# Performance work log

Measured on AMD Instinct MI355X. Metric: run time of the kernel, lower is better.

The kernel has to match this reference:

```python
import jax, jax.numpy as jnp
import numpy as np

N = 100000          # nodes
E = 1600000         # edges
DIMS = [128, 64, 64, 47]  # in_feats -> hidden -> hidden -> n_classes
EPS = 1e-5


def setup_inputs() -> dict:
    key = jax.random.key(0)
    ks = jax.random.split(key, 10)
    d = {
        "features": jax.random.normal(ks[0], (N, DIMS[0]), jnp.float32),
        "src": jax.random.randint(ks[1], (E,), 0, N, dtype=jnp.int64),
        "dst": jax.random.randint(ks[2], (E,), 0, N, dtype=jnp.int64),
    }
    # GraphConv weights (glorot-ish) + bias
    for i in range(3):
        fan_in, fan_out = DIMS[i], DIMS[i + 1]
        scale = jnp.sqrt(2.0 / (fan_in + fan_out)).astype(jnp.float32)
        d[f"W{i}"] = jax.random.normal(ks[3 + i], (fan_in, fan_out), jnp.float32) * scale
        d[f"b{i}"] = jnp.zeros((fan_out,), jnp.float32)
    # BatchNorm affine params for the first two layers
    for i in range(2):
        d[f"gamma{i}"] = jnp.ones((DIMS[i + 1],), jnp.float32)
        d[f"beta{i}"] = jnp.zeros((DIMS[i + 1],), jnp.float32)
    return d


def _degree_isqrt(idx):
    # clamp degree to >=1 like DGL, then D^{-1/2}
    deg = jax.ops.segment_sum(jnp.ones((E,), jnp.float32), idx, num_segments=N)
    return jax.lax.rsqrt(jnp.maximum(deg, 1.0))


def _graph_conv(h, W, b, src, dst, out_isqrt, in_isqrt):
    # DGL GraphConv, norm='both': h' = D_in^{-1/2} A D_out^{-1/2} h W + b
    h = h * out_isqrt[:, None]
    if W.shape[0] > W.shape[1]:  # mult W first when it shrinks features (DGL order)
        h = h @ W
        h = jax.ops.segment_sum(h[src], dst, num_segments=N)
    else:
        h = jax.ops.segment_sum(h[src], dst, num_segments=N)
        h = h @ W
    return h * in_isqrt[:, None] + b


def _batch_norm(h, gamma, beta):
    mu = h.mean(axis=0)
    var = h.var(axis=0)  # biased, as torch BatchNorm uses for normalization
    return gamma * (h - mu) * jax.lax.rsqrt(var + EPS) + beta


def reference(features, src, dst, W0, b0, W1, b1, W2, b2,
              gamma0, beta0, gamma1, beta1):
    out_isqrt = _degree_isqrt(src)
    in_isqrt = _degree_isqrt(dst)
    Ws = [(W0, b0), (W1, b1), (W2, b2)]
    bns = [(gamma0, beta0), (gamma1, beta1)]
    h = features
    for i, (W, b) in enumerate(Ws):
        # dropout (p=0.5) before last layer only -> identity in eval mode
        h = _graph_conv(h, W, b, src, dst, out_isqrt, in_isqrt)
        if i < len(Ws) - 1:
            h = _batch_norm(h, *bns[i])
            h = jax.nn.relu(h)
    return h
```

## Files before the change

kernel.cpp:

```cpp
#include <hip/hip_runtime.h>
#include <hip/hip_bf16.h>
#include <hip/hip_fp16.h>

#define BN_EPS 1e-5f
#define N_MAX 100000
#define CAP 64
#define NB_MAX 391
#define BCAP 8192

__device__ float g_wsf[130 * N_MAX + 256];
__device__ int   g_wsi[(1 + CAP) * N_MAX + NB_MAX * BCAP + 2 * NB_MAX + 64];
__device__ unsigned char g_wsb[NB_MAX * BCAP];

__global__ __launch_bounds__(256)
void k_bin(const int* __restrict__ src, const int* __restrict__ dst,
           int* __restrict__ gcur, int* __restrict__ scur,
           int* __restrict__ pairs, unsigned char* __restrict__ sbytes,
           int E, int nb) {
    __shared__ int dh[NB_MAX], db[NB_MAX], dc[NB_MAX];
    __shared__ int sh[NB_MAX], sb[NB_MAX], sc[NB_MAX];
    const int tid = threadIdx.x;
    for (int i = tid; i < nb; i += 256) { dh[i] = 0; sh[i] = 0; dc[i] = 0; sc[i] = 0; }
    __syncthreads();
    const int e0 = blockIdx.x * 4096;
    int ss[16], dd[16];
#pragma unroll
    for (int i = 0; i < 16; ++i) {
        int e = e0 + i * 256 + tid;
        if (e < E) {
            ss[i] = src[e]; dd[i] = dst[e];
            atomicAdd(&dh[dd[i] >> 8], 1);
            atomicAdd(&sh[ss[i] >> 8], 1);
        } else ss[i] = -1;
    }
    __syncthreads();
    for (int i = tid; i < nb; i += 256) {
        db[i] = atomicAdd(&gcur[i], dh[i]);
        sb[i] = atomicAdd(&scur[i], sh[i]);
    }
    __syncthreads();
#pragma unroll
    for (int i = 0; i < 16; ++i) {
        if (ss[i] >= 0) {
            int b = dd[i] >> 8;
            int idx = db[b] + atomicAdd(&dc[b], 1);
            if (idx < BCAP) pairs[b * BCAP + idx] = (ss[i] << 8) | (dd[i] & 255);
            int b2 = ss[i] >> 8;
            int i2 = sb[b2] + atomicAdd(&sc[b2], 1);
            if (i2 < BCAP) sbytes[b2 * BCAP + i2] = (unsigned char)(ss[i] & 255);
        }
    }
}

__global__ __launch_bounds__(256)
void k_slab(const int* __restrict__ gcur, const int* __restrict__ pairs,
            int* __restrict__ slab, int* __restrict__ cnt,
            float* __restrict__ isq_d, int n) {
    __shared__ int c[256];
    const int tid = threadIdx.x;
    const int d0 = blockIdx.x * 256;
    c[tid] = 0;
    __syncthreads();
    const int m = min(gcur[blockIdx.x], BCAP);
    const int base = blockIdx.x * BCAP;
    for (int i = tid; i < m; i += 256) {
        int p = pairs[base + i];
        int dl = p & 255;
        int slot = atomicAdd(&c[dl], 1);
        if (slot < CAP) slab[(size_t)(d0 + dl) * CAP + slot] = p >> 8;
    }
    __syncthreads();
    int d = d0 + tid;
    if (d < n) {
        cnt[d] = c[tid];
        isq_d[d] = rsqrtf(fmaxf((float)c[tid], 1.0f));
    }
}

__global__ __launch_bounds__(256)
void k_degs(const int* __restrict__ scur, const unsigned char* __restrict__ sbytes,
            float* __restrict__ isq_s, int n) {
    __shared__ int c[256];
    const int tid = threadIdx.x;
    c[tid] = 0;
    __syncthreads();
    const int m = min(scur[blockIdx.x], BCAP);
    const int base = blockIdx.x * BCAP;
    for (int i = tid; i < m; i += 256) atomicAdd(&c[sbytes[base + i]], 1);
    __syncthreads();
    int s = blockIdx.x * 256 + tid;
    if (s < n) isq_s[s] = rsqrtf(fmaxf((float)c[tid], 1.0f));
}

template<bool SB>
__global__ __launch_bounds__(256)
void k_agg(const int* __restrict__ cnt, const int* __restrict__ slab,
           const __half* __restrict__ in, const float* __restrict__ isq_d,
           const float* __restrict__ bias, float* __restrict__ out, int n) {
    const int d = (int)((blockIdx.x * 256u + threadIdx.x) >> 6);
    if (d >= n) return;
    const int lane = threadIdx.x & 63;
    const int sub = lane >> 3;
    const int fc = (lane & 7) << 3;
    const int m = min(cnt[d], CAP);
    const int* cs = slab + (size_t)d * CAP;
    float a0 = 0.0f, a1 = 0.0f, a2 = 0.0f, a3 = 0.0f;
    float a4 = 0.0f, a5 = 0.0f, a6 = 0.0f, a7 = 0.0f;
    for (int e = 0; e < m; e += 16) {
#pragma unroll
        for (int u = 0; u < 2; ++u) {
            int j = e + u * 8 + sub;
            if (j < m) {
                int s = cs[j];
                const uint4 v = *(const uint4*)(in + (size_t)s * 64 + fc);
                const float2 f0 = __half22float2(*(const __half2*)&v.x);
                const float2 f1 = __half22float2(*(const __half2*)&v.y);
                const float2 f2 = __half22float2(*(const __half2*)&v.z);
                const float2 f3 = __half22float2(*(const __half2*)&v.w);
                a0 += f0.x; a1 += f0.y; a2 += f1.x; a3 += f1.y;
                a4 += f2.x; a5 += f2.y; a6 += f3.x; a7 += f3.y;
            }
        }
    }
#pragma unroll
    for (int sh = 8; sh <= 32; sh <<= 1) {
        a0 += __shfl_xor(a0, sh); a1 += __shfl_xor(a1, sh);
        a2 += __shfl_xor(a2, sh); a3 += __shfl_xor(a3, sh);
        a4 += __shfl_xor(a4, sh); a5 += __shfl_xor(a5, sh);
        a6 += __shfl_xor(a6, sh); a7 += __shfl_xor(a7, sh);
    }
    if (sub == 0) {
        float4 r0, r1;
        if (SB) {
            const float sd = isq_d[d];
            const float4 b0 = *(const float4*)(bias + fc);
            const float4 b1 = *(const float4*)(bias + fc + 4);
            r0.x = a0 * sd + b0.x; r0.y = a1 * sd + b0.y;
            r0.z = a2 * sd + b0.z; r0.w = a3 * sd + b0.w;
            r1.x = a4 * sd + b1.x; r1.y = a5 * sd + b1.y;
            r1.z = a6 * sd + b1.z; r1.w = a7 * sd + b1.w;
        } else {
            r0.x = a0; r0.y = a1; r0.z = a2; r0.w = a3;
            r1.x = a4; r1.y = a5; r1.z = a6; r1.w = a7;
        }
        *(float4*)(out + (size_t)d * 64 + fc) = r0;
        *(float4*)(out + (size_t)d * 64 + fc + 4) = r1;
    }
}

template<int KIN, int KOUTR, bool BIAS, bool HOUT>
__global__ __launch_bounds__(256)
void k_gemm(const float* __restrict__ X, const float* __restrict__ rowscale,
            const float* __restrict__ W, const float* __restrict__ bias,
            float* __restrict__ C, int n) {
    __shared__ float Xs[KIN * 64];
    __shared__ float Ws[KIN * 64];
    const int tid = threadIdx.x;
    const int row0 = blockIdx.x * 64;
    {
        const int r = tid >> 2;
        const int row = row0 + r;
        const float sc = (row < n && rowscale) ? rowscale[row] : 1.0f;
        for (int kk = 0; kk < KIN; kk += 16) {
            const int k = kk + (tid & 3) * 4;
            float4 v = {0.0f, 0.0f, 0.0f, 0.0f};
            if (row < n) v = *(const float4*)(X + (size_t)row * KIN + k);
            Xs[(k + 0) * 64 + r] = v.x * sc;
            Xs[(k + 1) * 64 + r] = v.y * sc;
            Xs[(k + 2) * 64 + r] = v.z * sc;
            Xs[(k + 3) * 64 + r] = v.w * sc;
        }
    }
    for (int i = tid; i < KIN * 64; i += 256) {
        const int k = i >> 6, c = i & 63;
        Ws[i] = (c < KOUTR) ? W[k * KOUTR + c] : 0.0f;
    }
    __syncthreads();
    const int ty = tid >> 4;
    const int tx = tid & 15;
    float acc[4][4] = {};
#pragma unroll 2
    for (int k = 0; k < KIN; ++k) {
        const float4 a = *(const float4*)(Xs + k * 64 + ty * 4);
        const float4 b = *(const float4*)(Ws + k * 64 + tx * 4);
        acc[0][0] = fmaf(a.x, b.x, acc[0][0]); acc[0][1] = fmaf(a.x, b.y, acc[0][1]);
        acc[0][2] = fmaf(a.x, b.z, acc[0][2]); acc[0][3] = fmaf(a.x, b.w, acc[0][3]);
        acc[1][0] = fmaf(a.y, b.x, acc[1][0]); acc[1][1] = fmaf(a.y, b.y, acc[1][1]);
        acc[1][2] = fmaf(a.y, b.z, acc[1][2]); acc[1][3] = fmaf(a.y, b.w, acc[1][3]);
        acc[2][0] = fmaf(a.z, b.x, acc[2][0]); acc[2][1] = fmaf(a.z, b.y, acc[2][1]);
        acc[2][2] = fmaf(a.z, b.z, acc[2][2]); acc[2][3] = fmaf(a.z, b.w, acc[2][3]);
        acc[3][0] = fmaf(a.w, b.x, acc[3][0]); acc[3][1] = fmaf(a.w, b.y, acc[3][1]);
        acc[3][2] = fmaf(a.w, b.z, acc[3][2]); acc[3][3] = fmaf(a.w, b.w, acc[3][3]);
    }
#pragma unroll
    for (int i = 0; i < 4; ++i) {
        const int row = row0 + ty * 4 + i;
        if (row >= n) continue;
        if (KOUTR == 64) {
            float4 r;
            r.x = acc[i][0]; r.y = acc[i][1]; r.z = acc[i][2]; r.w = acc[i][3];
            if (BIAS) {
                const float4 b = *(const float4*)(bias + tx * 4);
                r.x += b.x; r.y += b.y; r.z += b.z; r.w += b.w;
            }
            if (HOUT) {
                __half2 h01 = __floats2half2_rn(r.x, r.y);
                __half2 h23 = __floats2half2_rn(r.z, r.w);
                uint2 u;
                u.x = *(const unsigned*)&h01;
                u.y = *(const unsigned*)&h23;
                *(uint2*)((__half*)C + (size_t)row * 64 + tx * 4) = u;
            } else {
                *(float4*)(C + (size_t)row * 64 + tx * 4) = r;
            }
        } else {
#pragma unroll
            for (int j = 0; j < 4; ++j) {
                const int c = tx * 4 + j;
                if (c < KOUTR)
                    C[(size_t)row * KOUTR + c] = BIAS ? acc[i][j] + bias[c] : acc[i][j];
            }
        }
    }
}

__global__ __launch_bounds__(256)
void k_bn_stats(const float* __restrict__ A, float* __restrict__ stats, int n) {
    const int f = threadIdx.x & 63;
    const int sub = threadIdx.x >> 6;
    float s = 0.0f, q = 0.0f;
    for (int i = blockIdx.x * 4 + sub; i < n; i += gridDim.x * 4) {
        float h = A[(size_t)i * 64 + f];
        s += h;
        q += h * h;
    }
    __shared__ float ls[4][64], lq[4][64];
    ls[sub][f] = s; lq[sub][f] = q;
    __syncthreads();
    if (sub == 0) {
        s = ls[0][f] + ls[1][f] + ls[2][f] + ls[3][f];
        q = lq[0][f] + lq[1][f] + lq[2][f] + lq[3][f];
        atomicAdd(&stats[f], s);
        atomicAdd(&stats[64 + f], q);
    }
}

__global__ __launch_bounds__(256)
void k_bn_apply(const float* __restrict__ A, const float* __restrict__ gamma,
                const float* __restrict__ beta, const float* __restrict__ stats,
                const float* __restrict__ outscale, __half* __restrict__ B, int n) {
    unsigned gid = blockIdx.x * 256u + threadIdx.x;
    unsigned i = gid >> 4;
    if (i >= (unsigned)n) return;
    unsigned fq = (gid & 15u) << 2;
    const float invn = 1.0f / (float)n;
    const float4 sm = *(const float4*)(stats + fq);
    const float4 sq = *(const float4*)(stats + 64 + fq);
    const float4 g  = *(const float4*)(gamma + fq);
    const float4 be = *(const float4*)(beta + fq);
    const float4 h  = *(const float4*)(A + (size_t)i * 64 + fq);
    const float os = outscale[i];
    float4 r;
    { float mu = sm.x * invn, var = sq.x * invn - mu * mu;
      r.x = fmaxf(g.x * (h.x - mu) * rsqrtf(var + BN_EPS) + be.x, 0.0f) * os; }
    { float mu = sm.y * invn, var = sq.y * invn - mu * mu;
      r.y = fmaxf(g.y * (h.y - mu) * rsqrtf(var + BN_EPS) + be.y, 0.0f) * os; }
    { float mu = sm.z * invn, var = sq.z * invn - mu * mu;
      r.z = fmaxf(g.z * (h.z - mu) * rsqrtf(var + BN_EPS) + be.z, 0.0f) * os; }
    { float mu = sm.w * invn, var = sq.w * invn - mu * mu;
      r.w = fmaxf(g.w * (h.w - mu) * rsqrtf(var + BN_EPS) + be.w, 0.0f) * os; }
    __half2 h01 = __floats2half2_rn(r.x, r.y);
    __half2 h23 = __floats2half2_rn(r.z, r.w);
    uint2 u;
    u.x = *(const unsigned*)&h01;
    u.y = *(const unsigned*)&h23;
    *(uint2*)(B + (size_t)i * 64 + fq) = u;
}

extern "C" void kernel_launch(void* const* d_in, const int* in_sizes, int n_in,
                              void* d_out, int out_size, void* d_ws, size_t ws_size,
                              hipStream_t stream) {
    const float* feat = (const float*)d_in[0];
    const int* src  = (const int*)d_in[1];
    const int* dst  = (const int*)d_in[2];
    const float* W0  = (const float*)d_in[3];
    const float* b0  = (const float*)d_in[4];
    const float* W1  = (const float*)d_in[5];
    const float* b1  = (const float*)d_in[6];
    const float* W2  = (const float*)d_in[7];
    const float* b2  = (const float*)d_in[8];
    const float* g0  = (const float*)d_in[9];
    const float* be0 = (const float*)d_in[10];
    const float* g1  = (const float*)d_in[11];
    const float* be1 = (const float*)d_in[12];

    const int n = out_size / 47;
    const int E = in_sizes[1];
    const int nb = (n + 255) >> 8;

    float* wsf = nullptr; int* wsi = nullptr; unsigned char* wsb = nullptr;
    hipGetSymbolAddress((void**)&wsf, HIP_SYMBOL(g_wsf));
    hipGetSymbolAddress((void**)&wsi, HIP_SYMBOL(g_wsi));
    hipGetSymbolAddress((void**)&wsb, HIP_SYMBOL(g_wsb));
    float* isq_s = wsf;
    float* isq_d = wsf + n;
    float* buf1  = wsf + 2 * (size_t)n;
    float* buf2  = buf1 + (size_t)n * 64;
    float* stats = buf2 + (size_t)n * 64;
    __half* buf1h = (__half*)buf1;
    __half* buf2h = (__half*)buf2;
    int* cnt     = wsi;
    int* slab    = wsi + n;
    int* pairs   = wsi + (size_t)(1 + CAP) * n;
    int* gcur    = pairs + (size_t)NB_MAX * BCAP;
    int* scur    = gcur + NB_MAX;

    const int gB = (E + 4095) / 4096;
    const int gW = (n + 3) / 4;
    const int gG = (n + 63) / 64;
    const int gA = (n * 16 + 255) / 256;

    hipMemsetAsync(gcur, 0, 2 * NB_MAX * sizeof(int), stream);
    hipMemsetAsync(stats, 0, 256 * sizeof(float), stream);
    k_bin<<<gB, 256, 0, stream>>>(src, dst, gcur, scur, pairs, wsb, E, nb);
    k_slab<<<nb, 256, 0, stream>>>(gcur, pairs, slab, cnt, isq_d, n);
    k_degs<<<nb, 256, 0, stream>>>(scur, wsb, isq_s, n);

    k_gemm<128, 64, false, true><<<gG, 256, 0, stream>>>(feat, isq_s, W0, nullptr, buf1, n);
    k_agg<true><<<gW, 256, 0, stream>>>(cnt, slab, buf1h, isq_d, b0, buf2, n);
    k_bn_stats<<<512, 256, 0, stream>>>(buf2, stats, n);
    k_bn_apply<<<gA, 256, 0, stream>>>(buf2, g0, be0, stats, isq_s, buf1h, n);

    k_agg<false><<<gW, 256, 0, stream>>>(cnt, slab, buf1h, nullptr, nullptr, buf2, n);
    k_gemm<64, 64, true, false><<<gG, 256, 0, stream>>>(buf2, isq_d, W1, b1, buf1, n);
    k_bn_stats<<<512, 256, 0, stream>>>(buf1, stats + 128, n);
    k_bn_apply<<<gA, 256, 0, stream>>>(buf1, g1, be1, stats + 128, isq_s, buf2h, n);

    k_agg<false><<<gW, 256, 0, stream>>>(cnt, slab, buf2h, nullptr, nullptr, buf1, n);
    k_gemm<64, 47, true, false><<<gG, 256, 0, stream>>>(buf1, isq_d, W2, b2, (float*)d_out, n);
}
```

Baseline: 496.8 us.

## Switch GEMMs to fp16 MFMA and store aggregation outputs in half precision

Replaces the scalar-FMA shared-memory GEMM with a kernel built on the 16x16x32 f16 MFMA instruction. It uses a swizzled LDS tile for the activations and keeps the weight fragments in registers. The aggregation kernel now writes fp16 instead of fp32, so the BN stats/apply and the following GEMM read half-width data. This cuts memory traffic and compute cost, at the price of extra fp16 rounding on intermediate activations and scalar (non-vectorized) output stores in the GEMM epilogue.

```diff
diff --git a/kernel.cpp b/kernel.cpp
--- a/kernel.cpp
+++ b/kernel.cpp
@@ -7,6 +7,9 @@
 #define CAP 64
 #define NB_MAX 391
 #define BCAP 8192
+
+typedef __attribute__((ext_vector_type(8))) _Float16 half8;
+typedef __attribute__((ext_vector_type(4))) float floatx4;
 
 __device__ float g_wsf[130 * N_MAX + 256];
 __device__ int   g_wsi[(1 + CAP) * N_MAX + NB_MAX * BCAP + 2 * NB_MAX + 64];
@@ -96,7 +99,7 @@
 __global__ __launch_bounds__(256)
 void k_agg(const int* __restrict__ cnt, const int* __restrict__ slab,
            const __half* __restrict__ in, const float* __restrict__ isq_d,
-           const float* __restrict__ bias, float* __restrict__ out, int n) {
+           const float* __restrict__ bias, __half* __restrict__ out, int n) {
     const int d = (int)((blockIdx.x * 256u + threadIdx.x) >> 6);
     if (d >= n) return;
     const int lane = threadIdx.x & 63;
@@ -130,107 +133,127 @@
         a6 += __shfl_xor(a6, sh); a7 += __shfl_xor(a7, sh);
     }
     if (sub == 0) {
-        float4 r0, r1;
         if (SB) {
             const float sd = isq_d[d];
             const float4 b0 = *(const float4*)(bias + fc);
             const float4 b1 = *(const float4*)(bias + fc + 4);
-            r0.x = a0 * sd + b0.x; r0.y = a1 * sd + b0.y;
-            r0.z = a2 * sd + b0.z; r0.w = a3 * sd + b0.w;
-            r1.x = a4 * sd + b1.x; r1.y = a5 * sd + b1.y;
-            r1.z = a6 * sd + b1.z; r1.w = a7 * sd + b1.w;
-        } else {
-            r0.x = a0; r0.y = a1; r0.z = a2; r0.w = a3;
-            r1.x = a4; r1.y = a5; r1.z = a6; r1.w = a7;
-        }
-        *(float4*)(out + (size_t)d * 64 + fc) = r0;
-        *(float4*)(out + (size_t)d * 64 + fc + 4) = r1;
-    }
-}
-
-template<int KIN, int KOUTR, bool BIAS, bool HOUT>
-__global__ __launch_bounds__(256)
-void k_gemm(const float* __restrict__ X, const float* __restrict__ rowscale,
-            const float* __restrict__ W, const float* __restrict__ bias,
-            float* __restrict__ C, int n) {
-    __shared__ float Xs[KIN * 64];
-    __shared__ float Ws[KIN * 64];
+            a0 = a0 * sd + b0.x; a1 = a1 * sd + b0.y;
+            a2 = a2 * sd + b0.z; a3 = a3 * sd + b0.w;
+            a4 = a4 * sd + b1.x; a5 = a5 * sd + b1.y;
+            a6 = a6 * sd + b1.z; a7 = a7 * sd + b1.w;
+        }
+        __half2 h01 = __floats2half2_rn(a0, a1);
+        __half2 h23 = __floats2half2_rn(a2, a3);
+        __half2 h45 = __floats2half2_rn(a4, a5);
+        __half2 h67 = __floats2half2_rn(a6, a7);
+        uint4 u;
+        u.x = *(const unsigned*)&h01; u.y = *(const unsigned*)&h23;
+        u.z = *(const unsigned*)&h45; u.w = *(const unsigned*)&h67;
+        *(uint4*)(out + (size_t)d * 64 + fc) = u;
+    }
+}
+
+template<int KIN, int KOUTR, bool HIN, bool HOUT, bool BIAS>
+__global__ __launch_bounds__(256)
+void k_gemm_mfma(const void* __restrict__ Xv, const float* __restrict__ rowscale,
+                 const float* __restrict__ W, const float* __restrict__ bias,
+                 void* __restrict__ Cv, int n) {
+    constexpr int NK = KIN / 32;
+    constexpr int NT = (KOUTR + 15) / 16;
+    constexpr int CHUNKS = KIN / 8;
+    __shared__ __align__(16) unsigned short Xs[64 * KIN];
     const int tid = threadIdx.x;
     const int row0 = blockIdx.x * 64;
-    {
-        const int r = tid >> 2;
-        const int row = row0 + r;
-        const float sc = (row < n && rowscale) ? rowscale[row] : 1.0f;
-        for (int kk = 0; kk < KIN; kk += 16) {
-            const int k = kk + (tid & 3) * 4;
-            float4 v = {0.0f, 0.0f, 0.0f, 0.0f};
-            if (row < n) v = *(const float4*)(X + (size_t)row * KIN + k);
-            Xs[(k + 0) * 64 + r] = v.x * sc;
-            Xs[(k + 1) * 64 + r] = v.y * sc;
-            Xs[(k + 2) * 64 + r] = v.z * sc;
-            Xs[(k + 3) * 64 + r] = v.w * sc;
-        }
-    }
-    for (int i = tid; i < KIN * 64; i += 256) {
-        const int k = i >> 6, c = i & 63;
-        Ws[i] = (c < KOUTR) ? W[k * KOUTR + c] : 0.0f;
-    }
-    __syncthreads();
-    const int ty = tid >> 4;
-    const int tx = tid & 15;
-    float acc[4][4] = {};
-#pragma unroll 2
-    for (int k = 0; k < KIN; ++k) {
-        const float4 a = *(const float4*)(Xs + k * 64 + ty * 4);
-        const float4 b = *(const float4*)(Ws + k * 64 + tx * 4);
-        acc[0][0] = fmaf(a.x, b.x, acc[0][0]); acc[0][1] = fmaf(a.x, b.y, acc[0][1]);
-        acc[0][2] = fmaf(a.x, b.z, acc[0][2]); acc[0][3] = fmaf(a.x, b.w, acc[0][3]);
-        acc[1][0] = fmaf(a.y, b.x, acc[1][0]); acc[1][1] = fmaf(a.y, b.y, acc[1][1]);
-        acc[1][2] = fmaf(a.y, b.z, acc[1][2]); acc[1][3] = fmaf(a.y, b.w, acc[1][3]);
-        acc[2][0] = fmaf(a.z, b.x, acc[2][0]); acc[2][1] = fmaf(a.z, b.y, acc[2][1]);
-        acc[2][2] = fmaf(a.z, b.z, acc[2][2]); acc[2][3] = fmaf(a.z, b.w, acc[2][3]);
-        acc[3][0] = fmaf(a.w, b.x, acc[3][0]); acc[3][1] = fmaf(a.w, b.y, acc[3][1]);
-        acc[3][2] = fmaf(a.w, b.z, acc[3][2]); acc[3][3] = fmaf(a.w, b.w, acc[3][3]);
-    }
-#pragma unroll
-    for (int i = 0; i < 4; ++i) {
-        const int row = row0 + ty * 4 + i;
-        if (row >= n) continue;
-        if (KOUTR == 64) {
-            float4 r;
-            r.x = acc[i][0]; r.y = acc[i][1]; r.z = acc[i][2]; r.w = acc[i][3];
-            if (BIAS) {
-                const float4 b = *(const float4*)(bias + tx * 4);
-                r.x += b.x; r.y += b.y; r.z += b.z; r.w += b.w;
+
+#pragma unroll
+    for (int it = 0; it < (64 * CHUNKS) / 256; ++it) {
+        const int idx = it * 256 + tid;
+        const int row = idx / CHUNKS;
+        const int ch = idx & (CHUNKS - 1);
+        const int rg = row0 + row;
+        uint4 v = {0u, 0u, 0u, 0u};
+        if (rg < n) {
+            if (HIN) {
+                v = *(const uint4*)((const __half*)Xv + (size_t)rg * KIN + ch * 8);
+            } else {
+                const float* Xf = (const float*)Xv;
+                const float4 f0 = *(const float4*)(Xf + (size_t)rg * KIN + ch * 8);
+                const float4 f1 = *(const float4*)(Xf + (size_t)rg * KIN + ch * 8 + 4);
+                __half2 h01 = __floats2half2_rn(f0.x, f0.y);
+                __half2 h23 = __floats2half2_rn(f0.z, f0.w);
+                __half2 h45 = __floats2half2_rn(f1.x, f1.y);
+                __half2 h67 = __floats2half2_rn(f1.z, f1.w);
+                v.x = *(const unsigned*)&h01; v.y = *(const unsigned*)&h23;
+                v.z = *(const unsigned*)&h45; v.w = *(const unsigned*)&h67;
             }
+        }
+        const int sch = ch ^ (row & 7);
+        *(uint4*)(&Xs[row * KIN + sch * 8]) = v;
+    }
+
+    const int lane = tid & 63;
+    const int lc = lane & 15;
+    const int lg = lane >> 4;
+    half8 bf[NK][NT];
+#pragma unroll
+    for (int s = 0; s < NK; ++s)
+#pragma unroll
+        for (int t = 0; t < NT; ++t)
+#pragma unroll
+            for (int j = 0; j < 8; ++j) {
+                const int k = s * 32 + lg * 8 + j;
+                const int c = t * 16 + lc;
+                const float wv = (c < KOUTR) ? W[k * KOUTR + c] : 0.0f;
+                bf[s][t][j] = (_Float16)wv;
+            }
+
+    __syncthreads();
+
+    const int w = tid >> 6;
+    const int rowl = 16 * w + lc;
+    floatx4 acc[NT];
+#pragma unroll
+    for (int t = 0; t < NT; ++t) acc[t] = 0.0f;
+#pragma unroll
+    for (int s = 0; s < NK; ++s) {
+        const int ch = s * 4 + lg;
+        const int sch = ch ^ (rowl & 7);
+        const half8 a = *(const half8*)(&Xs[rowl * KIN + sch * 8]);
+#pragma unroll
+        for (int t = 0; t < NT; ++t)
+            acc[t] = __builtin_amdgcn_mfma_f32_16x16x32_f16(a, bf[s][t], acc[t], 0, 0, 0);
+    }
+
+    const int rbase = row0 + 16 * w + lg * 4;
+#pragma unroll
+    for (int t = 0; t < NT; ++t) {
+        const int c = t * 16 + lc;
+#pragma unroll
+        for (int r = 0; r < 4; ++r) {
+            const int rg = rbase + r;
+            if (rg >= n) continue;
+            float v = acc[t][r] * rowscale[rg];
+            if (BIAS) v += bias[c];
             if (HOUT) {
-                __half2 h01 = __floats2half2_rn(r.x, r.y);
-                __half2 h23 = __floats2half2_rn(r.z, r.w);
-                uint2 u;
-                u.x = *(const unsigned*)&h01;
-                u.y = *(const unsigned*)&h23;
-                *(uint2*)((__half*)C + (size_t)row * 64 + tx * 4) = u;
+                ((__half*)Cv)[(size_t)rg * KOUTR + c] = __float2half_rn(v);
             } else {
-                *(float4*)(C + (size_t)row * 64 + tx * 4) = r;
+                if (KOUTR == 64 || c < KOUTR)
+                    ((float*)Cv)[(size_t)rg * KOUTR + c] = v;
             }
-        } else {
-#pragma unroll
-            for (int j = 0; j < 4; ++j) {
-                const int c = tx * 4 + j;
-                if (c < KOUTR)
-                    C[(size_t)row * KOUTR + c] = BIAS ? acc[i][j] + bias[c] : acc[i][j];
-            }
-        }
-    }
-}
-
-__global__ __launch_bounds__(256)
-void k_bn_stats(const float* __restrict__ A, float* __restrict__ stats, int n) {
+        }
+    }
+}
+
+template<bool HIN>
+__global__ __launch_bounds__(256)
+void k_bn_stats(const void* __restrict__ Av, float* __restrict__ stats, int n) {
     const int f = threadIdx.x & 63;
     const int sub = threadIdx.x >> 6;
     float s = 0.0f, q = 0.0f;
     for (int i = blockIdx.x * 4 + sub; i < n; i += gridDim.x * 4) {
-        float h = A[(size_t)i * 64 + f];
+        float h;
+        if (HIN) h = __half2float(((const __half*)Av)[(size_t)i * 64 + f]);
+        else     h = ((const float*)Av)[(size_t)i * 64 + f];
         s += h;
         q += h * h;
     }
@@ -245,8 +268,9 @@
     }
 }
 
-__global__ __launch_bounds__(256)
-void k_bn_apply(const float* __restrict__ A, const float* __restrict__ gamma,
+template<bool HIN>
+__global__ __launch_bounds__(256)
+void k_bn_apply(const void* __restrict__ Av, const float* __restrict__ gamma,
                 const float* __restrict__ beta, const float* __restrict__ stats,
                 const float* __restrict__ outscale, __half* __restrict__ B, int n) {
     unsigned gid = blockIdx.x * 256u + threadIdx.x;
@@ -258,7 +282,15 @@
     const float4 sq = *(const float4*)(stats + 64 + fq);
     const float4 g  = *(const float4*)(gamma + fq);
     const float4 be = *(const float4*)(beta + fq);
-    const float4 h  = *(const float4*)(A + (size_t)i * 64 + fq);
+    float4 h;
+    if (HIN) {
+        const uint2 u = *(const uint2*)((const __half*)Av + (size_t)i * 64 + fq);
+        const float2 p0 = __half22float2(*(const __half2*)&u.x);
+        const float2 p1 = __half22float2(*(const __half2*)&u.y);
+        h.x = p0.x; h.y = p0.y; h.z = p1.x; h.w = p1.y;
+    } else {
+        h = *(const float4*)((const float*)Av + (size_t)i * 64 + fq);
+    }
     const float os = outscale[i];
     float4 r;
     { float mu = sm.x * invn, var = sq.x * invn - mu * mu;
@@ -326,16 +358,16 @@
     k_slab<<<nb, 256, 0, stream>>>(gcur, pairs, slab, cnt, isq_d, n);
     k_degs<<<nb, 256, 0, stream>>>(scur, wsb, isq_s, n);
 
-    k_gemm<128, 64, false, true><<<gG, 256, 0, stream>>>(feat, isq_s, W0, nullptr, buf1, n);
-    k_agg<true><<<gW, 256, 0, stream>>>(cnt, slab, buf1h, isq_d, b0, buf2, n);
-    k_bn_stats<<<512, 256, 0, stream>>>(buf2, stats, n);
-    k_bn_apply<<<gA, 256, 0, stream>>>(buf2, g0, be0, stats, isq_s, buf1h, n);
-
-    k_agg<false><<<gW, 256, 0, stream>>>(cnt, slab, buf1h, nullptr, nullptr, buf2, n);
-    k_gemm<64, 64, true, false><<<gG, 256, 0, stream>>>(buf2, isq_d, W1, b1, buf1, n);
-    k_bn_stats<<<512, 256, 0, stream>>>(buf1, stats + 128, n);
-    k_bn_apply<<<gA, 256, 0, stream>>>(buf1, g1, be1, stats + 128, isq_s, buf2h, n);
-
-    k_agg<false><<<gW, 256, 0, stream>>>(cnt, slab, buf2h, nullptr, nullptr, buf1, n);
-    k_gemm<64, 47, true, false><<<gG, 256, 0, stream>>>(buf1, isq_d, W2, b2, (float*)d_out, n);
-}
+    k_gemm_mfma<128, 64, false, true, false><<<gG, 256, 0, stream>>>(feat, isq_s, W0, nullptr, buf1h, n);
+    k_agg<true><<<gW, 256, 0, stream>>>(cnt, slab, buf1h, isq_d, b0, buf2h, n);
+    k_bn_stats<true><<<512, 256, 0, stream>>>(buf2h, stats, n);
+    k_bn_apply<true><<<gA, 256, 0, stream>>>(buf2h, g0, be0, stats, isq_s, buf1h, n);
+
+    k_agg<false><<<gW, 256, 0, stream>>>(cnt, slab, buf1h, nullptr, nullptr, buf2h, n);
+    k_gemm_mfma<64, 64, true, false, true><<<gG, 256, 0, stream>>>(buf2h, isq_d, W1, b1, buf1, n);
+    k_bn_stats<false><<<512, 256, 0, stream>>>(buf1, stats + 128, n);
+    k_bn_apply<false><<<gA, 256, 0, stream>>>(buf1, g1, be1, stats + 128, isq_s, buf2h, n);
+
+    k_agg<false><<<gW, 256, 0, stream>>>(cnt, slab, buf2h, nullptr, nullptr, buf1h, n);
+    k_gemm_mfma<64, 47, true, false, true><<<gG, 256, 0, stream>>>(buf1h, isq_d, W2, b2, (float*)d_out, n);
+}
```

After: 468.2 us. -5.7%, faster.
